# Kernel tuning notes

Measured on AMD Instinct MI355X. Metric: run time of the kernel, lower is better.

## Reference

```python
import jax, jax.numpy as jnp
import numpy as np

B, L, D_MODEL = 4, 2048, 256
D_STATE, D_CONV, EXPAND = 16, 4, 2
D_INNER = EXPAND * D_MODEL          # 512
DT_RANK = (D_MODEL + 15) // 16      # 16
HORIZON = 96


def setup_inputs() -> dict:
    key = jax.random.key(0)
    ks = jax.random.split(key, 8)
    s = lambda k, shape, scale=0.02: jax.random.normal(k, shape, dtype=jnp.float32) * scale
    return {
        "x": jax.random.normal(ks[0], (B, L, D_MODEL), dtype=jnp.float32),
        "in_proj_w": s(ks[1], (2 * D_INNER, D_MODEL)),          # no bias (mamba default)
        "conv_w": s(ks[2], (D_INNER, 1, D_CONV), 0.1),          # depthwise causal conv
        "conv_b": jnp.zeros((D_INNER,), jnp.float32),
        "x_proj_w": s(ks[3], (DT_RANK + 2 * D_STATE, D_INNER)),
        "dt_proj_w": s(ks[4], (D_INNER, DT_RANK), 0.1),
        # softplus^{-1}(0.01): typical small initial dt
        "dt_proj_b": jnp.log(jnp.expm1(jnp.full((D_INNER,), 0.01, jnp.float32))),
        "A_log": jnp.log(jnp.broadcast_to(jnp.arange(1, D_STATE + 1, dtype=jnp.float32), (D_INNER, D_STATE))),
        "D_param": jnp.ones((D_INNER,), jnp.float32),
        "out_proj_w": s(ks[5], (D_MODEL, D_INNER)),
        "head_w": s(ks[6], (HORIZON, D_MODEL)),
        "head_b": jnp.zeros((HORIZON,), jnp.float32),
    }


def _silu(x):
    return x * jax.nn.sigmoid(x)


def _forward(x, in_proj_w, conv_w, conv_b, x_proj_w, dt_proj_w, dt_proj_b,
             A_log, D_param, out_proj_w, head_w, head_b):
    # in_proj -> split into conv/ssm branch and gate z
    xz = x @ in_proj_w.T                      # (B, L, 2*d_inner)
    x_in, z = jnp.split(xz, 2, axis=-1)
    # depthwise causal conv over time
    x_t = jnp.transpose(x_in, (0, 2, 1))      # (B, d_inner, L)
    x_conv = jax.lax.conv_general_dilated(
        x_t, conv_w, (1,), [(D_CONV - 1, 0)],
        feature_group_count=D_INNER, dimension_numbers=("NCH", "OIH", "NCH"))
    u = _silu(jnp.transpose(x_conv + conv_b[None, :, None], (0, 2, 1)))  # (B, L, d_inner)
    # input-dependent dt, B, C
    x_dbl = u @ x_proj_w.T
    dt, Bm, Cm = jnp.split(x_dbl, [DT_RANK, DT_RANK + D_STATE], axis=-1)
    delta = jax.nn.softplus(dt @ dt_proj_w.T + dt_proj_b)  # (B, L, d_inner)
    A = -jnp.exp(A_log)                                     # (d_inner, d_state)
    deltaA = jnp.exp(delta[..., None] * A)                  # (B, L, d_inner, d_state)
    deltaBu = delta[..., None] * Bm[:, :, None, :] * u[..., None]

    def step(h, ins):
        dA, dBu, c = ins                                    # (B,d,n),(B,d,n),(B,n)
        h = dA * h + dBu
        y = jnp.einsum("bdn,bn->bd", h, c)
        return h, y

    h0 = jnp.zeros((x.shape[0], D_INNER, D_STATE), x.dtype)
    xs = (jnp.moveaxis(deltaA, 1, 0), jnp.moveaxis(deltaBu, 1, 0), jnp.moveaxis(Cm, 1, 0))
    _, ys = jax.lax.scan(step, h0, xs)                      # (L, B, d_inner)
    y = jnp.moveaxis(ys, 0, 1) + u * D_param
    y = y * _silu(z)
    out = y @ out_proj_w.T                                  # (B, L, d_model)
    last = out[:, -1, :]
    return last @ head_w.T + head_b                         # (B, HORIZON)


def reference(x, in_proj_w, conv_w, conv_b, x_proj_w, dt_proj_w, dt_proj_b,
              A_log, D_param, out_proj_w, head_w, head_b):
    return _forward(x, in_proj_w, conv_w, conv_b, x_proj_w, dt_proj_w, dt_proj_b,
                    A_log, D_param, out_proj_w, head_w, head_b)
```

## Files before the change

### kernel.cpp

```cpp
#include <hip/hip_runtime.h>
#include <math.h>

#define BATCH 4
#define LSEQ 2048
#define BL (BATCH*LSEQ)
#define DMODEL 256
#define DINNER 512
#define NSTATE 16
#define DTRANK 16
#define NPROJ 48
#define HORIZ 96
#define NCH 32
#define TCH (LSEQ/NCH)

typedef __attribute__((ext_vector_type(8))) short short8b;
typedef __attribute__((ext_vector_type(4))) short short4b;
typedef __attribute__((ext_vector_type(4))) float f32x4;

__device__ __forceinline__ unsigned short f2bf(float f) {
  unsigned u = __float_as_uint(f);
  u += 0x7FFF + ((u >> 16) & 1);
  return (unsigned short)(u >> 16);
}
__device__ __forceinline__ float bf2f(unsigned short h) {
  return __uint_as_float(((unsigned)h) << 16);
}

__global__ __launch_bounds__(512) void k_front(const float* __restrict__ X,
                                               const float* __restrict__ W,
                                               const float* __restrict__ cw,
                                               const float* __restrict__ cb,
                                               const float* __restrict__ xpw,
                                               const float* __restrict__ opw,
                                               const float* __restrict__ hw,
                                               float* __restrict__ uT,
                                               float* __restrict__ dbl,
                                               float* __restrict__ hwf) {
  __shared__ unsigned short sBX[48 * 264];
  __shared__ unsigned short sw2[48 * 136];
  __shared__ float u_lds[128 * 36];
  const int tid = threadIdx.x;
  const int btc = blockIdx.x;
  if (btc >= 256) {
    const int fid = btc - 256;
    const int k0 = fid * 8;
    float* scratch = u_lds;
    {
      int m = tid >> 1;
      int half = (tid & 1) << 2;
      *(float4*)&scratch[m * 8 + half] =
        *(const float4*)&opw[(size_t)m * DINNER + k0 + half];
    }
    __syncthreads();
    for (int u = tid; u < HORIZ * 8; u += 512) {
      int t = u >> 3, kk = u & 7;
      const float* hr = &hw[(size_t)t * DMODEL];
      float acc = 0.f;
      #pragma unroll 8
      for (int m = 0; m < DMODEL; ++m) acc = fmaf(hr[m], scratch[m*8 + kk], acc);
      hwf[(size_t)t * DINNER + k0 + kk] = acc;
    }
    return;
  }
  const int bt0 = btc * 32;
  const bool edge0 = ((bt0 & (LSEQ - 1)) == 0);
  const int lane = tid & 63;
  const int w  = tid >> 6;
  const int fl = lane & 15;
  const int fg = lane >> 4;
  for (int u = tid; u < 1536; u += 512) {
    int tok = u >> 5, ko = u & 31;
    int g = bt0 - 16 + tok;
    if (g < 0) g = 0;
    const float* xr = &X[(size_t)g * DMODEL + ko * 8];
    float4 a = *(const float4*)xr, b = *(const float4*)(xr + 4);
    unsigned short t8[8] = {f2bf(a.x), f2bf(a.y), f2bf(a.z), f2bf(a.w),
                            f2bf(b.x), f2bf(b.y), f2bf(b.z), f2bf(b.w)};
    *(short8b*)&sBX[tok * 264 + ko * 8] = *(short8b*)t8;
  }
  float facc[4] = {0.f, 0.f, 0.f, 0.f};
  const int xo = tid >> 3;
  const int xt = (tid & 7) * 4;
  const int sj = tid >> 2;
  const int sk = tid & 3;
  for (int jc = 0; jc < 4; ++jc) {
    const int jbase = jc * 128;
    __syncthreads();
    for (int u = tid; u < 1536; u += 512) {
      int o = u >> 5, k4 = (u & 31) * 4;
      float4 v = *(const float4*)&xpw[(size_t)o * DINNER + jbase + k4];
      unsigned short t4[4] = {f2bf(v.x), f2bf(v.y), f2bf(v.z), f2bf(v.w)};
      *(short4b*)&sw2[o * 136 + k4] = *(short4b*)t4;
    }
    short8b aw[8];
    {
      const float* wrow = &W[(size_t)(jbase + w * 16 + fl) * DMODEL + fg * 8];
      #pragma unroll
      for (int ks = 0; ks < 8; ++ks) {
        float4 a = *(const float4*)(wrow + ks * 32);
        float4 b = *(const float4*)(wrow + ks * 32 + 4);
        unsigned short t8[8] = {f2bf(a.x), f2bf(a.y), f2bf(a.z), f2bf(a.w),
                                f2bf(b.x), f2bf(b.y), f2bf(b.z), f2bf(b.w)};
        aw[ks] = *(short8b*)t8;
      }
    }
    f32x4 acc0 = {0,0,0,0}, acc1 = {0,0,0,0}, acc2 = {0,0,0,0};
    #pragma unroll
    for (int ks = 0; ks < 8; ++ks) {
      const int kcol = (ks * 4 + fg) * 8;
      short8b x0 = *(short8b*)&sBX[(fl)      * 264 + kcol];
      short8b x1 = *(short8b*)&sBX[(16 + fl) * 264 + kcol];
      short8b x2 = *(short8b*)&sBX[(32 + fl) * 264 + kcol];
      acc0 = __builtin_amdgcn_mfma_f32_16x16x32_bf16(x0, aw[ks], acc0, 0, 0, 0);
      acc1 = __builtin_amdgcn_mfma_f32_16x16x32_bf16(x1, aw[ks], acc1, 0, 0, 0);
      acc2 = __builtin_amdgcn_mfma_f32_16x16x32_bf16(x2, aw[ks], acc2, 0, 0, 0);
    }
    if (edge0) acc0 = (f32x4){0,0,0,0};
    const int j = jbase + w * 16 + fl;
    const float4 cwv = *(const float4*)&cw[j * 4];
    const float cbv = cb[j];
    float u1[4], u2[4];
    {
      float s3a = __shfl(acc1[3], lane - 16), s3b = __shfl(acc0[3], lane + 48);
      float s2a = __shfl(acc1[2], lane - 16), s2b = __shfl(acc0[2], lane + 48);
      float s1a = __shfl(acc1[1], lane - 16), s1b = __shfl(acc0[1], lane + 48);
      float p1 = fg ? s3a : s3b, p2 = fg ? s2a : s2b, p3 = fg ? s1a : s1b;
      float xm1[4] = {p1, acc1[0], acc1[1], acc1[2]};
      float xm2[4] = {p2, p1, acc1[0], acc1[1]};
      float xm3[4] = {p3, p2, p1, acc1[0]};
      #pragma unroll
      for (int r = 0; r < 4; ++r) {
        float s = cbv;
        s = fmaf(cwv.x, xm3[r], s); s = fmaf(cwv.y, xm2[r], s);
        s = fmaf(cwv.z, xm1[r], s); s = fmaf(cwv.w, acc1[r], s);
        u1[r] = s / (1.f + __expf(-s));
      }
    }
    {
      float s3a = __shfl(acc2[3], lane - 16), s3b = __shfl(acc1[3], lane + 48);
      float s2a = __shfl(acc2[2], lane - 16), s2b = __shfl(acc1[2], lane + 48);
      float s1a = __shfl(acc2[1], lane - 16), s1b = __shfl(acc1[1], lane + 48);
      float p1 = fg ? s3a : s3b, p2 = fg ? s2a : s2b, p3 = fg ? s1a : s1b;
      float xm1[4] = {p1, acc2[0], acc2[1], acc2[2]};
      float xm2[4] = {p2, p1, acc2[0], acc2[1]};
      float xm3[4] = {p3, p2, p1, acc2[0]};
      #pragma unroll
      for (int r = 0; r < 4; ++r) {
        float s = cbv;
        s = fmaf(cwv.x, xm3[r], s); s = fmaf(cwv.y, xm2[r], s);
        s = fmaf(cwv.z, xm1[r], s); s = fmaf(cwv.w, acc2[r], s);
        u2[r] = s / (1.f + __expf(-s));
      }
    }
    {
      const int jl = w * 16 + fl;
      #pragma unroll
      for (int r = 0; r < 4; ++r) {
        u_lds[jl * 36 + fg * 4 + r]      = u1[r];
        u_lds[jl * 36 + 16 + fg * 4 + r] = u2[r];
      }
    }
    __syncthreads();
    {
      const int tq = sk * 8;
      float4 a = *(float4*)&u_lds[sj * 36 + tq];
      float4 b = *(float4*)&u_lds[sj * 36 + tq + 4];
      *(float4*)&uT[(size_t)(jbase + sj) * BL + bt0 + tq]     = a;
      *(float4*)&uT[(size_t)(jbase + sj) * BL + bt0 + tq + 4] = b;
    }
    if (tid < 384) {
      #pragma unroll 4
      for (int k = 0; k < 128; ++k) {
        float wv = bf2f(sw2[xo * 136 + k]);
        float4 uv = *(float4*)&u_lds[k * 36 + xt];
        facc[0] = fmaf(uv.x, wv, facc[0]);
        facc[1] = fmaf(uv.y, wv, facc[1]);
        facc[2] = fmaf(uv.z, wv, facc[2]);
        facc[3] = fmaf(uv.w, wv, facc[3]);
      }
    }
  }
  if (tid < 384) {
    #pragma unroll
    for (int i = 0; i < 4; ++i)
      dbl[(size_t)(bt0 + xt + i) * NPROJ + xo] = facc[i];
  }
}

__global__ __launch_bounds__(256) void k_scan(const float* __restrict__ uT,
                                              const float* __restrict__ dbl,
                                              const float* __restrict__ dtw,
                                              const float* __restrict__ dtb,
                                              const float* __restrict__ Alog,
                                              float* __restrict__ aprod,
                                              float* __restrict__ hacc) {
  __shared__ float sdt[64][17];
  __shared__ float sB[64][16];
  __shared__ float sdp[16][66][2];
  __shared__ float su[16][68];
  __shared__ float sdtw[16][17];
  __shared__ float sdtb[16];
  const int dblk = blockIdx.x, c = blockIdx.y, b = blockIdx.z;
  const int tid = threadIdx.x;
  const int d0 = dblk * 16;
  const int bt0 = b * LSEQ + c * TCH;
  {
    int tok = tid >> 2, q = (tid & 3) << 2;
    float4 v = *(const float4*)&dbl[(size_t)(bt0 + tok) * NPROJ + q];
    sdt[tok][q] = v.x; sdt[tok][q + 1] = v.y; sdt[tok][q + 2] = v.z; sdt[tok][q + 3] = v.w;
    float4 ww = *(const float4*)&dbl[(size_t)(bt0 + tok) * NPROJ + DTRANK + q];
    *(float4*)&sB[tok][q] = ww;
    int dl = tid >> 4, tq = (tid & 15) << 2;
    *(float4*)&su[dl][tq] = *(const float4*)&uT[(size_t)(d0 + dl) * BL + bt0 + tq];
    sdtw[tid >> 4][tid & 15] = dtw[(d0 + (tid >> 4)) * DTRANK + (tid & 15)];
    if (tid < 16) sdtb[tid] = dtb[d0 + tid];
  }
  __syncthreads();
  {
    int tok = tid >> 2, dl4 = (tid & 3) << 2;
    #pragma unroll
    for (int dd = 0; dd < 4; ++dd) {
      int dl = dl4 + dd;
      float a = sdtb[dl];
      #pragma unroll
      for (int r = 0; r < DTRANK; ++r) a = fmaf(sdt[tok][r], sdtw[dl][r], a);
      float dlt = (a > 20.f) ? a : log1pf(__expf(a));
      sdp[dl][tok][0] = dlt;
      sdp[dl][tok][1] = dlt * su[dl][tok];
    }
  }
  __syncthreads();
  const int dl = tid >> 4, n = tid & 15;
  const int d = d0 + dl;
  const float A = -__expf(Alog[d * NSTATE + n]);
  float ap = 1.f, h = 0.f;
  #pragma unroll 8
  for (int tt = 0; tt < TCH; ++tt) {
    float2 dp = *(const float2*)&sdp[dl][tt][0];
    float dA = __expf(dp.x * A);
    h = fmaf(dA, h, dp.y * sB[tt][n]);
    ap *= dA;
  }
  size_t off = (((size_t)b * NCH + c) * DINNER + d) * NSTATE + n;
  aprod[off] = ap;
  hacc[off] = h;
}

__global__ __launch_bounds__(256) void k_combine(const float* __restrict__ aprod,
                                                 const float* __restrict__ hacc,
                                                 const float* __restrict__ dbl,
                                                 const float* __restrict__ uT,
                                                 const float* __restrict__ Dp,
                                                 const float* __restrict__ X,
                                                 const float* __restrict__ ipw,
                                                 float* __restrict__ ybuf) {
  __shared__ float sx[DMODEL];
  const int dblk = blockIdx.x & 31, b = blockIdx.x >> 5;
  const int tid = threadIdx.x;
  const int dl = tid >> 4, n = tid & 15;
  const int d = dblk * 16 + dl;
  sx[tid] = X[((size_t)b * LSEQ + LSEQ - 1) * DMODEL + tid];
  float h = 0.f;
  for (int c = 0; c < NCH; ++c) {
    size_t off = (((size_t)b * NCH + c) * DINNER + d) * NSTATE + n;
    h = fmaf(aprod[off], h, hacc[off]);
  }
  __syncthreads();
  float zp = 0.f;
  {
    const float* zr = &ipw[(size_t)(DINNER + d) * DMODEL + (n << 4)];
    #pragma unroll
    for (int q = 0; q < 4; ++q) {
      float4 w4 = *(const float4*)&zr[q << 2];
      float4 x4 = *(const float4*)&sx[(n << 4) + (q << 2)];
      zp = fmaf(w4.x, x4.x, zp); zp = fmaf(w4.y, x4.y, zp);
      zp = fmaf(w4.z, x4.z, zp); zp = fmaf(w4.w, x4.w, zp);
    }
  }
  const int btL = b * LSEQ + LSEQ - 1;
  float Cv = dbl[(size_t)btL * NPROJ + DTRANK + NSTATE + n];
  float v = h * Cv;
  #pragma unroll
  for (int off = 1; off < 16; off <<= 1) {
    v  += __shfl_xor(v, off);
    zp += __shfl_xor(zp, off);
  }
  if (n == 0) {
    float y = v + uT[(size_t)d * BL + btL] * Dp[d];
    ybuf[b * DINNER + d] = y * zp / (1.f + __expf(-zp));
  }
}

__global__ __launch_bounds__(256) void k_out(const float* __restrict__ sy,
                                             const float* __restrict__ hwf,
                                             const float* __restrict__ hb,
                                             float* __restrict__ out) {
  const int t = blockIdx.x;
  const int b = threadIdx.x >> 6;
  const int lane = threadIdx.x & 63;
  const int k0 = lane << 3;
  const float* yr = &sy[(size_t)b * DINNER + k0];
  const float* wr = &hwf[(size_t)t * DINNER + k0];
  float4 y0 = *(const float4*)yr, y1 = *(const float4*)(yr + 4);
  float4 w0 = *(const float4*)wr, w1 = *(const float4*)(wr + 4);
  float s = y0.x * w0.x + y0.y * w0.y + y0.z * w0.z + y0.w * w0.w
          + y1.x * w1.x + y1.y * w1.y + y1.z * w1.z + y1.w * w1.w;
  #pragma unroll
  for (int off = 1; off < 64; off <<= 1) s += __shfl_xor(s, off);
  if (lane == 0) out[b * HORIZ + t] = s + hb[t];
}

extern "C" void kernel_launch(void* const* d_in, const int* in_sizes, int n_in,
                              void* d_out, int out_size, void* d_ws, size_t ws_size,
                              hipStream_t stream) {
  (void)in_sizes; (void)n_in; (void)out_size; (void)ws_size;
  const float* x    = (const float*)d_in[0];
  const float* ipw  = (const float*)d_in[1];
  const float* cw   = (const float*)d_in[2];
  const float* cb   = (const float*)d_in[3];
  const float* xpw  = (const float*)d_in[4];
  const float* dtw  = (const float*)d_in[5];
  const float* dtb  = (const float*)d_in[6];
  const float* Alog = (const float*)d_in[7];
  const float* Dp   = (const float*)d_in[8];
  const float* opw  = (const float*)d_in[9];
  const float* hw   = (const float*)d_in[10];
  const float* hb   = (const float*)d_in[11];
  float* out = (float*)d_out;
  float* ws  = (float*)d_ws;

  float* uT    = ws;
  float* dbl   = ws + 4194304;
  float* aprod = ws + 4587520;
  float* hacc  = ws + 5636096;
  float* ybuf  = ws + 6684672;
  float* hwf   = ws + 6686720;

  k_front<<<320, 512, 0, stream>>>(x, ipw, cw, cb, xpw, opw, hw, uT, dbl, hwf);
  k_scan<<<dim3(32, NCH, BATCH), 256, 0, stream>>>(uT, dbl, dtw, dtb, Alog, aprod, hacc);
  k_combine<<<128, 256, 0, stream>>>(aprod, hacc, dbl, uT, Dp, x, ipw, ybuf);
  k_out<<<HORIZ, 256, 0, stream>>>(ybuf, hwf, hb, out);
}
```

Before: 75.62 us.

## Split k_front d_inner range across two blocks with partial x_proj sums

Each 32-token tile of k_front is now handled by two blocks, each covering half of the d_inner channels. The x_proj output becomes two partial sums written to separate buffers, which k_scan and k_combine add together when loading. The x_proj weights are also kept in fp32 in LDS, so the bf16 round-trip is dropped. This doubles the grid (256 to 512 main blocks) to fill more CUs on MI355X. In exchange, the tokens' halo X load and bf16 conversion are repeated per block, and partial-sum traffic and workspace grow.

```diff
diff --git a/kernel.cpp b/kernel.cpp
--- a/kernel.cpp
+++ b/kernel.cpp
@@ -12,18 +12,15 @@
 #define HORIZ 96
 #define NCH 32
 #define TCH (LSEQ/NCH)
+#define PSTRIDE (BL*NPROJ)
 
 typedef __attribute__((ext_vector_type(8))) short short8b;
-typedef __attribute__((ext_vector_type(4))) short short4b;
 typedef __attribute__((ext_vector_type(4))) float f32x4;
 
 __device__ __forceinline__ unsigned short f2bf(float f) {
   unsigned u = __float_as_uint(f);
   u += 0x7FFF + ((u >> 16) & 1);
   return (unsigned short)(u >> 16);
-}
-__device__ __forceinline__ float bf2f(unsigned short h) {
-  return __uint_as_float(((unsigned)h) << 16);
 }
 
 __global__ __launch_bounds__(512) void k_front(const float* __restrict__ X,
@@ -34,15 +31,15 @@
                                                const float* __restrict__ opw,
                                                const float* __restrict__ hw,
                                                float* __restrict__ uT,
-                                               float* __restrict__ dbl,
+                                               float* __restrict__ part,
                                                float* __restrict__ hwf) {
   __shared__ unsigned short sBX[48 * 264];
-  __shared__ unsigned short sw2[48 * 136];
+  __shared__ float sw2[48 * 132];
   __shared__ float u_lds[128 * 36];
   const int tid = threadIdx.x;
-  const int btc = blockIdx.x;
-  if (btc >= 256) {
-    const int fid = btc - 256;
+  const int bx = blockIdx.x;
+  if (bx >= 512) {
+    const int fid = bx - 512;
     const int k0 = fid * 8;
     float* scratch = u_lds;
     {
@@ -62,6 +59,8 @@
     }
     return;
   }
+  const int btc = bx >> 1;
+  const int jp  = bx & 1;
   const int bt0 = btc * 32;
   const bool edge0 = ((bt0 & (LSEQ - 1)) == 0);
   const int lane = tid & 63;
@@ -83,14 +82,12 @@
   const int xt = (tid & 7) * 4;
   const int sj = tid >> 2;
   const int sk = tid & 3;
-  for (int jc = 0; jc < 4; ++jc) {
-    const int jbase = jc * 128;
+  for (int jc = 0; jc < 2; ++jc) {
+    const int jbase = jp * 256 + jc * 128;
     __syncthreads();
     for (int u = tid; u < 1536; u += 512) {
-      int o = u >> 5, k4 = (u & 31) * 4;
-      float4 v = *(const float4*)&xpw[(size_t)o * DINNER + jbase + k4];
-      unsigned short t4[4] = {f2bf(v.x), f2bf(v.y), f2bf(v.z), f2bf(v.w)};
-      *(short4b*)&sw2[o * 136 + k4] = *(short4b*)t4;
+      int o = u >> 5, k4 = (u & 31) << 2;
+      *(float4*)&sw2[o * 132 + k4] = *(const float4*)&xpw[(size_t)o * DINNER + jbase + k4];
     }
     short8b aw[8];
     {
@@ -171,7 +168,7 @@
     if (tid < 384) {
       #pragma unroll 4
       for (int k = 0; k < 128; ++k) {
-        float wv = bf2f(sw2[xo * 136 + k]);
+        float wv = sw2[xo * 132 + k];
         float4 uv = *(float4*)&u_lds[k * 36 + xt];
         facc[0] = fmaf(uv.x, wv, facc[0]);
         facc[1] = fmaf(uv.y, wv, facc[1]);
@@ -183,12 +180,12 @@
   if (tid < 384) {
     #pragma unroll
     for (int i = 0; i < 4; ++i)
-      dbl[(size_t)(bt0 + xt + i) * NPROJ + xo] = facc[i];
+      part[(size_t)jp * PSTRIDE + (size_t)(bt0 + xt + i) * NPROJ + xo] = facc[i];
   }
 }
 
 __global__ __launch_bounds__(256) void k_scan(const float* __restrict__ uT,
-                                              const float* __restrict__ dbl,
+                                              const float* __restrict__ part,
                                               const float* __restrict__ dtw,
                                               const float* __restrict__ dtb,
                                               const float* __restrict__ Alog,
@@ -206,9 +203,14 @@
   const int bt0 = b * LSEQ + c * TCH;
   {
     int tok = tid >> 2, q = (tid & 3) << 2;
-    float4 v = *(const float4*)&dbl[(size_t)(bt0 + tok) * NPROJ + q];
-    sdt[tok][q] = v.x; sdt[tok][q + 1] = v.y; sdt[tok][q + 2] = v.z; sdt[tok][q + 3] = v.w;
-    float4 ww = *(const float4*)&dbl[(size_t)(bt0 + tok) * NPROJ + DTRANK + q];
+    size_t base = (size_t)(bt0 + tok) * NPROJ + q;
+    float4 v0 = *(const float4*)&part[base];
+    float4 v1 = *(const float4*)&part[base + PSTRIDE];
+    sdt[tok][q] = v0.x + v1.x; sdt[tok][q + 1] = v0.y + v1.y;
+    sdt[tok][q + 2] = v0.z + v1.z; sdt[tok][q + 3] = v0.w + v1.w;
+    float4 w0 = *(const float4*)&part[base + DTRANK];
+    float4 w1 = *(const float4*)&part[base + DTRANK + PSTRIDE];
+    float4 ww = make_float4(w0.x + w1.x, w0.y + w1.y, w0.z + w1.z, w0.w + w1.w);
     *(float4*)&sB[tok][q] = ww;
     int dl = tid >> 4, tq = (tid & 15) << 2;
     *(float4*)&su[dl][tq] = *(const float4*)&uT[(size_t)(d0 + dl) * BL + bt0 + tq];
@@ -248,7 +250,7 @@
 
 __global__ __launch_bounds__(256) void k_combine(const float* __restrict__ aprod,
                                                  const float* __restrict__ hacc,
-                                                 const float* __restrict__ dbl,
+                                                 const float* __restrict__ part,
                                                  const float* __restrict__ uT,
                                                  const float* __restrict__ Dp,
                                                  const float* __restrict__ X,
@@ -278,7 +280,8 @@
     }
   }
   const int btL = b * LSEQ + LSEQ - 1;
-  float Cv = dbl[(size_t)btL * NPROJ + DTRANK + NSTATE + n];
+  size_t cbase = (size_t)btL * NPROJ + DTRANK + NSTATE + n;
+  float Cv = part[cbase] + part[cbase + PSTRIDE];
   float v = h * Cv;
   #pragma unroll
   for (int off = 1; off < 16; off <<= 1) {
@@ -330,14 +333,14 @@
   float* ws  = (float*)d_ws;
 
   float* uT    = ws;
-  float* dbl   = ws + 4194304;
-  float* aprod = ws + 4587520;
-  float* hacc  = ws + 5636096;
-  float* ybuf  = ws + 6684672;
-  float* hwf   = ws + 6686720;
-
-  k_front<<<320, 512, 0, stream>>>(x, ipw, cw, cb, xpw, opw, hw, uT, dbl, hwf);
-  k_scan<<<dim3(32, NCH, BATCH), 256, 0, stream>>>(uT, dbl, dtw, dtb, Alog, aprod, hacc);
-  k_combine<<<128, 256, 0, stream>>>(aprod, hacc, dbl, uT, Dp, x, ipw, ybuf);
+  float* part  = ws + 4194304;
+  float* aprod = ws + 4980736;
+  float* hacc  = ws + 6029312;
+  float* ybuf  = ws + 7077888;
+  float* hwf   = ws + 7079936;
+
+  k_front<<<576, 512, 0, stream>>>(x, ipw, cw, cb, xpw, opw, hw, uT, part, hwf);
+  k_scan<<<dim3(32, NCH, BATCH), 256, 0, stream>>>(uT, part, dtw, dtb, Alog, aprod, hacc);
+  k_combine<<<128, 256, 0, stream>>>(aprod, hacc, part, uT, Dp, x, ipw, ybuf);
   k_out<<<HORIZ, 256, 0, stream>>>(ybuf, hwf, hb, out);
 }
```

Result: no change. 76.16 us (+0.7%).
